# Performance work log

Hardware: AMD Instinct MI355X
Metric: run time of the kernel (lower is better)

The kernel has to match this reference:

```python
import jax, jax.numpy as jnp
import numpy as np

NUM_GROUPS = 32
EPS = 1e-6


def group_norm(x, scale, bias):
    # x: (b, c, t, h, w)
    b, c, t, h, w = x.shape
    xg = x.reshape(b, NUM_GROUPS, c // NUM_GROUPS, t, h, w)
    mean = jnp.mean(xg, axis=(2, 3, 4, 5), keepdims=True)
    var = jnp.var(xg, axis=(2, 3, 4, 5), keepdims=True)
    xg = (xg - mean) * jax.lax.rsqrt(var + EPS)
    xn = xg.reshape(b, c, t, h, w)
    return xn * scale[None, :, None, None, None] + bias[None, :, None, None, None]


def conv1x1(x, w, bvec):
    # 1x1x1 Conv3d == per-position linear over channels
    return jnp.einsum('oc,bcthw->bothw', w, x) + bvec[None, :, None, None, None]


def setup_inputs() -> dict:
    key = jax.random.key(0)
    ks = jax.random.split(key, 11)
    b, c, t, h, w = 2, 256, 4, 32, 32
    x = jax.random.normal(ks[0], (b, c, t, h, w), dtype=jnp.float32)
    s = 1.0 / np.sqrt(c)
    return {
        'x': x,
        'gn_scale': jnp.ones((c,), jnp.float32),
        'gn_bias': jnp.zeros((c,), jnp.float32),
        'wq': jax.random.normal(ks[1], (c, c), jnp.float32) * s,
        'bq': jax.random.normal(ks[2], (c,), jnp.float32) * 0.01,
        'wk': jax.random.normal(ks[3], (c, c), jnp.float32) * s,
        'bk': jax.random.normal(ks[4], (c,), jnp.float32) * 0.01,
        'wv': jax.random.normal(ks[5], (c, c), jnp.float32) * s,
        'bv': jax.random.normal(ks[6], (c,), jnp.float32) * 0.01,
        'wp': jax.random.normal(ks[7], (c, c), jnp.float32) * s,
        'bp': jax.random.normal(ks[8], (c,), jnp.float32) * 0.01,
    }


def reference(x, gn_scale, gn_bias, wq, bq, wk, bk, wv, bv, wp, bp):
    b, c, t, h, w = x.shape
    n = t * h * w
    h_ = group_norm(x, gn_scale, gn_bias)
    q = conv1x1(h_, wq, bq).reshape(b, c, n)  # (b, c, n)
    k = conv1x1(h_, wk, bk).reshape(b, c, n)
    v = conv1x1(h_, wv, bv).reshape(b, c, n)
    scale = jnp.asarray(int(c) ** (-0.5), x.dtype)
    # attn[b, i, j] = sum_c q[b,c,i] k[b,c,j]
    attn = jnp.einsum('bci,bcj->bij', q, k) * scale
    attn = jax.nn.softmax(attn, axis=2)
    # A[b, c, i] = sum_j v[b,c,j] attn[b,i,j]
    A = jnp.einsum('bcj,bij->bci', v, attn).reshape(b, c, t, h, w)
    A = conv1x1(A, wp, bp)
    return x + A
```

## Files before the change

### kernel.cpp

```cpp
#include <hip/hip_runtime.h>
#include <hip/hip_bf16.h>
#include <math.h>

#define BB 2
#define CC 256
#define GG 32
#define NN 4096
#define EPSF 1e-6f
#define JSPLIT 8
#define JBLK (NN / JSPLIT)
#define CH 32
#define NT (JBLK / CH)
#define QTILE 128
#define ITILE 32
#define LOG2E 1.4426950408889634f

typedef _Float16 f16x8 __attribute__((ext_vector_type(8)));
typedef float f32x4 __attribute__((ext_vector_type(4)));
typedef float f32x16 __attribute__((ext_vector_type(16)));

static __device__ __forceinline__ unsigned short f2h_bits(float f) {
    _Float16 h = (_Float16)f;
    return __builtin_bit_cast(unsigned short, h);
}
static __device__ __forceinline__ unsigned pkh2(float a, float b) {
    return __builtin_bit_cast(unsigned, __builtin_amdgcn_cvt_pkrtz(a, b));
}
static __device__ __forceinline__ void gload16(const void* g, void* l) {
    __builtin_amdgcn_global_load_lds(
        (const __attribute__((address_space(1))) void*)g,
        (__attribute__((address_space(3))) void*)l, 16, 0, 0);
}

__global__ __launch_bounds__(256) void prep_gn_kernel(
    const float* __restrict__ wq, const float* __restrict__ wk,
    const float* __restrict__ wv, const float* __restrict__ wp,
    unsigned short* __restrict__ w16,
    const float* __restrict__ x, float2* __restrict__ part)
{
    __shared__ float red[8];
    int id = blockIdx.x;
    int t  = threadIdx.x;
    if (id < 256) {
        int m = id >> 6;
        const float* src = (m == 0) ? wq : (m == 1) ? wk : (m == 2) ? wv : wp;
        float scale = (m == 0) ? 0.0625f * LOG2E : 1.0f;
        int idx = (id & 63) * 256 + t;
        float4 v = ((const float4*)src)[idx];
        union { _Float16 h[4]; uint2 u; } pk;
        pk.h[0] = (_Float16)(v.x * scale);
        pk.h[1] = (_Float16)(v.y * scale);
        pk.h[2] = (_Float16)(v.z * scale);
        pk.h[3] = (_Float16)(v.w * scale);
        *(uint2*)(w16 + (size_t)m * CC * CC + (size_t)idx * 4) = pk.u;
    } else {
        int rem = id - 256;
        int g = rem & 31, p = (rem >> 5) & 3, b = rem >> 7;
        const float* base = x + ((size_t)b * CC + (size_t)g * 8) * NN + (size_t)p * 8192;
        float s = 0.f, ss = 0.f;
        for (int idx = t; idx < 2048; idx += 256) {
            float4 v4 = ((const float4*)base)[idx];
            s  += v4.x + v4.y + v4.z + v4.w;
            ss += v4.x*v4.x + v4.y*v4.y + v4.z*v4.z + v4.w*v4.w;
        }
        for (int off = 32; off; off >>= 1) {
            s  += __shfl_down(s,  off);
            ss += __shfl_down(ss, off);
        }
        int wid = t >> 6;
        if ((t & 63) == 0) { red[wid*2] = s; red[wid*2+1] = ss; }
        __syncthreads();
        if (t == 0) {
            part[(b*GG + g)*4 + p] = make_float2(red[0]+red[2]+red[4]+red[6],
                                                 red[1]+red[3]+red[5]+red[7]);
        }
    }
}

__global__ __launch_bounds__(256) void proj_qkv_kernel(
    const float* __restrict__ x, const float* __restrict__ sc,
    const float* __restrict__ bi, const float2* __restrict__ part,
    const unsigned short* __restrict__ w16,
    const float* __restrict__ bq, const float* __restrict__ bk,
    const float* __restrict__ bv,
    unsigned short* __restrict__ qT, unsigned short* __restrict__ kT,
    unsigned short* __restrict__ vC)
{
    int b  = blockIdx.y;
    int i0 = blockIdx.x * 32;
    int t  = threadIdx.x;
    __shared__ unsigned short htile[32 * 256];
    __shared__ float s_mean[GG], s_rstd[GG], s_sc[CC], s_bi[CC];
    if (t < GG) {
        float2 p0 = part[(b*GG + t)*4 + 0];
        float2 p1 = part[(b*GG + t)*4 + 1];
        float2 p2 = part[(b*GG + t)*4 + 2];
        float2 p3 = part[(b*GG + t)*4 + 3];
        float S  = p0.x + p1.x + p2.x + p3.x;
        float SS = p0.y + p1.y + p2.y + p3.y;
        float mean = S / 32768.f;
        float var  = SS / 32768.f - mean * mean;
        s_mean[t] = mean;
        s_rstd[t] = rsqrtf(var + EPSF);
    }
    s_sc[t] = sc[t];
    s_bi[t] = bi[t];
    __syncthreads();

    char* hw = (char*)htile;
    int nq = (t & 7) * 4;
    int cq = (t >> 3) * 4;
    #pragma unroll
    for (int k = 0; k < 2; k++) {
        int c0 = cq + k * 128;
        float4 xr[4];
        float aa[4], dd[4];
        #pragma unroll
        for (int e = 0; e < 4; e++) {
            int c = c0 + e;
            xr[e] = *(const float4*)(x + ((size_t)b*CC + c)*NN + i0 + nq);
            aa[e] = s_rstd[c >> 3] * s_sc[c];
            dd[e] = s_bi[c] - s_mean[c >> 3] * aa[e];
        }
        #pragma unroll
        for (int j = 0; j < 4; j++) {
            int row = nq + j;
            union { _Float16 h[4]; uint2 u; } pk;
            pk.h[0] = (_Float16)(((const float*)&xr[0])[j] * aa[0] + dd[0]);
            pk.h[1] = (_Float16)(((const float*)&xr[1])[j] * aa[1] + dd[1]);
            pk.h[2] = (_Float16)(((const float*)&xr[2])[j] * aa[2] + dd[2]);
            pk.h[3] = (_Float16)(((const float*)&xr[3])[j] * aa[3] + dd[3]);
            int off = row*512 + (((c0 >> 3) ^ (row & 7)) << 4) + (c0 & 7) * 2;
            *(uint2*)(hw + off) = pk.u;
        }
    }
    __syncthreads();

    int lane = t & 63, w = t >> 6;
    int col = lane & 15, grp = lane >> 4;
    const char* hr = (const char*)htile;

    #pragma unroll
    for (int p = 0; p < 2; p++) {
        const unsigned short* wgt = w16 + (size_t)p * CC * CC;
        const float* bias = p ? bk : bq;
        unsigned short* outp = (p ? kT : qT) + (size_t)b * NN * CC;
        float osc = p ? 1.0f : 0.0625f * LOG2E;
        #pragma unroll
        for (int ot = 0; ot < 4; ot++) {
            int ow = ot * 64 + w * 16;
            f32x4 acc[2];
            acc[0] = (f32x4){0.f,0.f,0.f,0.f};
            acc[1] = (f32x4){0.f,0.f,0.f,0.f};
            #pragma unroll
            for (int ck = 0; ck < 8; ck++) {
                f16x8 af = *(const f16x8*)(wgt + (size_t)(ow + col)*CC + ck*32 + grp*8);
                #pragma unroll
                for (int it = 0; it < 2; it++) {
                    int row = it*16 + col;
                    f16x8 bf = *(const f16x8*)(hr + row*512 + (((ck*4 + grp) ^ (row & 7)) << 4));
                    acc[it] = __builtin_amdgcn_mfma_f32_16x16x32_f16(af, bf, acc[it], 0, 0, 0);
                }
            }
            int obase = ow + grp * 4;
            float b0 = bias[obase]*osc, b1 = bias[obase+1]*osc,
                  b2 = bias[obase+2]*osc, b3 = bias[obase+3]*osc;
            #pragma unroll
            for (int it = 0; it < 2; it++) {
                int i = i0 + it*16 + col;
                union { _Float16 h[4]; uint2 u; } pk;
                pk.h[0] = (_Float16)(acc[it][0] + b0);
                pk.h[1] = (_Float16)(acc[it][1] + b1);
                pk.h[2] = (_Float16)(acc[it][2] + b2);
                pk.h[3] = (_Float16)(acc[it][3] + b3);
                *(uint2*)(outp + (size_t)i*CC + obase) = pk.u;
            }
        }
    }
    {
        const unsigned short* wgt = w16 + (size_t)2 * CC * CC;
        unsigned short* outp = vC + (size_t)b * CC * NN;
        int ibase = (w & 1) * 16;
        #pragma unroll
        for (int gg = 0; gg < 2; gg++) {
            int og = (w >> 1) * 2 + gg;
            f32x4 acc[4];
            #pragma unroll
            for (int ot = 0; ot < 4; ot++) acc[ot] = (f32x4){0.f,0.f,0.f,0.f};
            #pragma unroll
            for (int ck = 0; ck < 8; ck++) {
                int row = ibase + col;
                f16x8 af = *(const f16x8*)(hr + row*512 + (((ck*4 + grp) ^ (row & 7)) << 4));
                #pragma unroll
                for (int ot = 0; ot < 4; ot++) {
                    f16x8 bf = *(const f16x8*)(wgt + (size_t)(og*64 + ot*16 + col)*CC + ck*32 + grp*8);
                    acc[ot] = __builtin_amdgcn_mfma_f32_16x16x32_f16(af, bf, acc[ot], 0, 0, 0);
                }
            }
            int iw = i0 + ibase + grp * 4;
            #pragma unroll
            for (int ot = 0; ot < 4; ot++) {
                int o = og*64 + ot*16 + col;
                float bo = bv[o];
                union { _Float16 h[4]; uint2 u; } pk;
                pk.h[0] = (_Float16)(acc[ot][0] + bo);
                pk.h[1] = (_Float16)(acc[ot][1] + bo);
                pk.h[2] = (_Float16)(acc[ot][2] + bo);
                pk.h[3] = (_Float16)(acc[ot][3] + bo);
                *(uint2*)(outp + (size_t)o*NN + iw) = pk.u;
            }
        }
    }
}

#define STAGE_K(tt, bb) do { int _j = jlo + (tt)*CH; _Pragma("unroll") \
    for (int e = 0; e < 4; e++) gload16(kb + (size_t)_j*CC + koff[e], &bufK[bb][(4*w + e)*512]); } while (0)
#define STAGE_V(tt, bb) do { int _j = jlo + (tt)*CH; _Pragma("unroll") \
    for (int e = 0; e < 4; e++) gload16(vb + voff[e] + _j, &bufV[bb][(4*w + e)*512]); } while (0)

__global__ __launch_bounds__(256, 2) void attn_kernel(
    const unsigned short* __restrict__ qT,
    const unsigned short* __restrict__ kT,
    const unsigned short* __restrict__ vC,
    unsigned short* __restrict__ pO,
    float2* __restrict__ ml)
{
    int qt = blockIdx.x, s = blockIdx.y, b = blockIdx.z;
    int tid = threadIdx.x, w = tid >> 6, lane = tid & 63;
    int l31 = lane & 31, hi = lane >> 5;
    int col = lane & 15, grp = lane >> 4;
    int q0 = qt * QTILE + w * 32;
    int jlo = s * JBLK;

    __shared__ __align__(16) unsigned short bufK[2][8192];
    __shared__ __align__(16) unsigned short bufV[2][8192];
    __shared__ __align__(16) unsigned short plds[4 * 1280];

    const unsigned short* qb = qT + (size_t)b * NN * CC;
    const unsigned short* kb = kT + (size_t)b * NN * CC;
    const unsigned short* vb = vC + (size_t)b * CC * NN;

    f16x8 qf[16];
    #pragma unroll
    for (int ck = 0; ck < 16; ck++)
        qf[ck] = *(const f16x8*)(qb + (size_t)(q0 + l31)*CC + ck*16 + hi*8);

    int koff[4], voff[4];
    #pragma unroll
    for (int e = 0; e < 4; e++) {
        int blk = (4*w + e)*64 + lane;
        int kj = blk >> 5, kcb = blk & 31;
        koff[e] = kj*CC + ((kcb ^ (kj & 7)) * 8);
        int vc = blk >> 2, vcb = blk & 3;
        voff[e] = vc*NN + ((vcb ^ ((vc >> 1) & 3)) * 8);
    }
    int kru = l31 * 512;
    int kx  = l31 & 7;
    int vrb = col*64 + ((grp ^ ((col >> 1) & 3)) << 4);
    char* pw  = (char*)plds + w*2560 + l31*80 + 8*hi;
    const char* prd = (const char*)plds + w*2560;

    f32x4 O0[16], O1[16];
    #pragma unroll
    for (int ct = 0; ct < 16; ct++) {
        O0[ct] = (f32x4){0.f,0.f,0.f,0.f};
        O1[ct] = (f32x4){0.f,0.f,0.f,0.f};
    }
    float m = -1e30f, l = 0.f;

    STAGE_K(0, 0);
    STAGE_V(0, 0);
    __syncthreads();

    for (int t = 0; t < NT; t++) {
        int cur = t & 1;
        if (t + 1 < NT) {
            STAGE_K(t + 1, cur ^ 1);
            STAGE_V(t + 1, cur ^ 1);
        }
        const char* kbase = (const char*)&bufK[cur][0];
        const char* vbase = (const char*)&bufV[cur][0];

        f32x16 S;
        #pragma unroll
        for (int r = 0; r < 16; r++) S[r] = 0.f;
        __builtin_amdgcn_s_setprio(1);
        #pragma unroll
        for (int ck = 0; ck < 16; ck++) {
            f16x8 kf = *(const f16x8*)(kbase + kru + ((((ck*2) | hi) ^ kx) << 4));
            S = __builtin_amdgcn_mfma_f32_32x32x16_f16(kf, qf[ck], S, 0, 0, 0);
        }
        __builtin_amdgcn_s_setprio(0);

        float x0 = fmaxf(fmaxf(S[0], S[1]), fmaxf(S[2], S[3]));
        float x1 = fmaxf(fmaxf(S[4], S[5]), fmaxf(S[6], S[7]));
        float x2 = fmaxf(fmaxf(S[8], S[9]), fmaxf(S[10], S[11]));
        float x3 = fmaxf(fmaxf(S[12], S[13]), fmaxf(S[14], S[15]));
        float mh = fmaxf(fmaxf(x0, x1), fmaxf(x2, x3));
        float mx = fmaxf(mh, __shfl_xor(mh, 32));

        if (!__all(mx <= m + 8.f)) {
            float mn = fmaxf(m, mx);
            float f = exp2f(m - mn);
            m = mn;
            l *= f;
            float fq0 = __shfl(f, col);
            float fq1 = __shfl(f, 16 + col);
            #pragma unroll
            for (int ct = 0; ct < 16; ct++) { O0[ct] *= fq0; O1[ct] *= fq1; }
        }

        #pragma unroll
        for (int r = 0; r < 16; r++) S[r] = exp2f(S[r] - m);
        float ps = (((S[0]+S[1]) + (S[2]+S[3])) + ((S[4]+S[5]) + (S[6]+S[7])))
                 + (((S[8]+S[9]) + (S[10]+S[11])) + ((S[12]+S[13]) + (S[14]+S[15])));
        l += ps + __shfl_xor(ps, 32);

        {
            unsigned* pr = (unsigned*)pw;
            pr[0]  = pkh2(S[0],  S[1]);   pr[1]  = pkh2(S[2],  S[3]);
            pr[4]  = pkh2(S[4],  S[5]);   pr[5]  = pkh2(S[6],  S[7]);
            pr[8]  = pkh2(S[8],  S[9]);   pr[9]  = pkh2(S[10], S[11]);
            pr[12] = pkh2(S[12], S[13]);  pr[13] = pkh2(S[14], S[15]);
        }
        asm volatile("s_waitcnt lgkmcnt(0)" ::: "memory");
        __builtin_amdgcn_sched_barrier(0);

        f16x8 y0 = *(const f16x8*)(prd + col*80 + grp*16);
        f16x8 y1 = *(const f16x8*)(prd + (16 + col)*80 + grp*16);
        __builtin_amdgcn_s_setprio(1);
        #pragma unroll
        for (int ct = 0; ct < 16; ct++) {
            f16x8 xf = *(const f16x8*)(vbase + ct*1024 + vrb);
            O0[ct] = __builtin_amdgcn_mfma_f32_16x16x32_f16(xf, y0, O0[ct], 0, 0, 0);
            O1[ct] = __builtin_amdgcn_mfma_f32_16x16x32_f16(xf, y1, O1[ct], 0, 0, 0);
        }
        __builtin_amdgcn_s_setprio(0);
        __syncthreads();
    }

    float inv = 1.f / l;
    float iq0 = __shfl(inv, col);
    float iq1 = __shfl(inv, 16 + col);
    unsigned short* po = pO + ((size_t)(s*BB + b)*NN + q0) * CC;
    #pragma unroll
    for (int ct = 0; ct < 16; ct++) {
        int c = ct*16 + grp*4;
        *(unsigned*)(po + (size_t)col*CC + c)            = pkh2(O0[ct][0]*iq0, O0[ct][1]*iq0);
        *(unsigned*)(po + (size_t)col*CC + c + 2)        = pkh2(O0[ct][2]*iq0, O0[ct][3]*iq0);
        *(unsigned*)(po + (size_t)(16 + col)*CC + c)     = pkh2(O1[ct][0]*iq1, O1[ct][1]*iq1);
        *(unsigned*)(po + (size_t)(16 + col)*CC + c + 2) = pkh2(O1[ct][2]*iq1, O1[ct][3]*iq1);
    }
    if (lane < 32)
        ml[(size_t)(s*BB + b)*NN + q0 + lane] = make_float2(m, l);
}

__global__ __launch_bounds__(256, 2) void proj_out_merge_kernel(
    const unsigned short* __restrict__ pO, const float2* __restrict__ ml,
    const unsigned short* __restrict__ wp16, const float* __restrict__ bp,
    const float* __restrict__ x, float* __restrict__ out)
{
    int b  = blockIdx.y;
    int i0 = blockIdx.x * ITILE;
    int t  = threadIdx.x;
    __shared__ __align__(16) unsigned short htile[ITILE * 256];

    {
        int row  = t >> 3;
        int cseg = (t & 7) * 32;
        size_t qrow = (size_t)b * NN + i0 + row;
        float M = -1e30f;
        float m8[JSPLIT], l8[JSPLIT];
        #pragma unroll
        for (int s = 0; s < JSPLIT; s++) {
            float2 v = ml[(size_t)s*BB*NN + qrow];
            m8[s] = v.x; l8[s] = v.y;
            M = fmaxf(M, v.x);
        }
        float W = 0.f, wt[JSPLIT];
        #pragma unroll
        for (int s = 0; s < JSPLIT; s++) { wt[s] = l8[s] * exp2f(m8[s] - M); W += wt[s]; }
        float iW = 1.f / W;
        float acc[32];
        #pragma unroll
        for (int e = 0; e < 32; e++) acc[e] = 0.f;
        #pragma unroll
        for (int s = 0; s < JSPLIT; s++) {
            const unsigned short* p = pO + ((size_t)s*BB*NN + qrow)*CC + cseg;
            float ws = wt[s] * iW;
            #pragma unroll
            for (int k = 0; k < 4; k++) {
                f16x8 a = *(const f16x8*)(p + k*8);
                #pragma unroll
                for (int e = 0; e < 8; e++) acc[k*8 + e] += ws * (float)a[e];
            }
        }
        char* hw = (char*)htile;
        #pragma unroll
        for (int k = 0; k < 4; k++) {
            int c0 = cseg + k*8;
            uint4 pk;
            pk.x = pkh2(acc[k*8+0], acc[k*8+1]);
            pk.y = pkh2(acc[k*8+2], acc[k*8+3]);
            pk.z = pkh2(acc[k*8+4], acc[k*8+5]);
            pk.w = pkh2(acc[k*8+6], acc[k*8+7]);
            int off = row*512 + (((c0 >> 3) ^ (row & 7)) << 4);
            *(uint4*)(hw + off) = pk;
        }
    }
    __syncthreads();

    int lane = t & 63, wid = t >> 6;
    int col = lane & 15, grp = lane >> 4;
    int rl0 = (wid & 1) * 16;
    int ibase = i0 + rl0;
    const char* hr = (const char*)htile;
    #pragma unroll
    for (int gg = 0; gg < 2; gg++) {
        int o0 = ((wid >> 1) * 2 + gg) * 64;
        f32x4 acc[4];
        #pragma unroll
        for (int ot = 0; ot < 4; ot++) acc[ot] = (f32x4){0.f,0.f,0.f,0.f};
        #pragma unroll
        for (int ck = 0; ck < 8; ck++) {
            int rl = rl0 + col;
            f16x8 af = *(const f16x8*)(hr + rl*512 + (((ck*4 + grp) ^ (rl & 7)) << 4));
            #pragma unroll
            for (int ot = 0; ot < 4; ot++) {
                f16x8 bf = *(const f16x8*)(wp16 + (size_t)(o0 + ot*16 + col)*CC + ck*32 + grp*8);
                acc[ot] = __builtin_amdgcn_mfma_f32_16x16x32_f16(af, bf, acc[ot], 0, 0, 0);
            }
        }
        int iw = ibase + grp * 4;
        #pragma unroll
        for (int ot = 0; ot < 4; ot++) {
            int o = o0 + ot*16 + col;
            float bo = bp[o];
            size_t base = (size_t)b*CC*NN + (size_t)o*NN + iw;
            float4 x4 = *(const float4*)(x + base);
            float4 r;
            r.x = x4.x + acc[ot][0] + bo;
            r.y = x4.y + acc[ot][1] + bo;
            r.z = x4.z + acc[ot][2] + bo;
            r.w = x4.w + acc[ot][3] + bo;
            *(float4*)(out + base) = r;
        }
    }
}

extern "C" void kernel_launch(void* const* d_in, const int* in_sizes, int n_in,
                              void* d_out, int out_size, void* d_ws, size_t ws_size,
                              hipStream_t stream) {
    const float* x  = (const float*)d_in[0];
    const float* gs = (const float*)d_in[1];
    const float* gb = (const float*)d_in[2];
    const float* wq = (const float*)d_in[3];
    const float* bq = (const float*)d_in[4];
    const float* wk = (const float*)d_in[5];
    const float* bk = (const float*)d_in[6];
    const float* wv = (const float*)d_in[7];
    const float* bv = (const float*)d_in[8];
    const float* wp = (const float*)d_in[9];
    const float* bp = (const float*)d_in[10];
    float* out = (float*)d_out;

    char* ws = (char*)d_ws;
    const size_t sz = (size_t)BB * NN * CC * sizeof(unsigned short);
    unsigned short* qT  = (unsigned short*)(ws + sz);
    unsigned short* kT  = (unsigned short*)(ws + 2*sz);
    unsigned short* vC  = (unsigned short*)(ws + 3*sz);
    unsigned short* w16 = (unsigned short*)(ws + 5*sz);
    float2* part        = (float2*)(ws + 5*sz + 512*1024);
    float2* ml          = (float2*)(ws + 5*sz + 768*1024);
    unsigned short* pO  = (unsigned short*)(ws + 5*sz + 1280*1024);

    prep_gn_kernel<<<dim3(512), 256, 0, stream>>>(wq, wk, wv, wp, w16, x, part);
    proj_qkv_kernel<<<dim3(NN/32, BB), 256, 0, stream>>>(x, gs, gb, part, w16,
                                                         bq, bk, bv, qT, kT, vC);
    attn_kernel<<<dim3(NN/QTILE, JSPLIT, BB), 256, 0, stream>>>(qT, kT, vC, pO, ml);
    proj_out_merge_kernel<<<dim3(NN/ITILE, BB), 256, 0, stream>>>(pO, ml, w16 + 3*CC*CC,
                                                                  bp, x, out);
}
```

Measured before the change: 116.9 us.

## Software-pipeline QK^T one tile ahead with triple-buffered K in attention

The attention kernel now uses 512 threads per block covering a 256-row query tile, so each block's staged K/V tiles feed twice as many query rows and each thread issues half as many async loads. K is triple-buffered and V double-buffered. The QK^T MFMA for tile t+1 is computed before the softmax and PV of tile t, so matrix work overlaps the softmax and the global-to-LDS waits. Explicit vmcnt waits and raw s_barrier calls replace __syncthreads. The costs are more registers (S2 is held live alongside the O accumulators), more LDS per block and fewer blocks in the grid, which may reduce occupancy on the chip.

```diff
diff --git a/kernel.cpp b/kernel.cpp
--- a/kernel.cpp
+++ b/kernel.cpp
@@ -11,7 +11,7 @@
 #define JBLK (NN / JSPLIT)
 #define CH 32
 #define NT (JBLK / CH)
-#define QTILE 128
+#define QTILE 256
 #define ITILE 32
 #define LOG2E 1.4426950408889634f
 
@@ -31,6 +31,9 @@
         (const __attribute__((address_space(1))) void*)g,
         (__attribute__((address_space(3))) void*)l, 16, 0, 0);
 }
+#define WAITV(n) asm volatile("s_waitcnt vmcnt(" #n ")" ::: "memory")
+#define SBAR() do { __builtin_amdgcn_sched_barrier(0); __builtin_amdgcn_s_barrier(); \
+                    __builtin_amdgcn_sched_barrier(0); } while (0)
 
 __global__ __launch_bounds__(256) void prep_gn_kernel(
     const float* __restrict__ wq, const float* __restrict__ wk,
@@ -214,11 +217,17 @@
 }
 
 #define STAGE_K(tt, bb) do { int _j = jlo + (tt)*CH; _Pragma("unroll") \
-    for (int e = 0; e < 4; e++) gload16(kb + (size_t)_j*CC + koff[e], &bufK[bb][(4*w + e)*512]); } while (0)
+    for (int e = 0; e < 2; e++) gload16(kb + (size_t)_j*CC + koff[e], &bufK[bb][(2*w + e)*512]); } while (0)
 #define STAGE_V(tt, bb) do { int _j = jlo + (tt)*CH; _Pragma("unroll") \
-    for (int e = 0; e < 4; e++) gload16(vb + voff[e] + _j, &bufV[bb][(4*w + e)*512]); } while (0)
-
-__global__ __launch_bounds__(256, 2) void attn_kernel(
+    for (int e = 0; e < 2; e++) gload16(vb + voff[e] + _j, &bufV[bb][(2*w + e)*512]); } while (0)
+#define QK_INTO(dst, kn) do { \
+    _Pragma("unroll") for (int r = 0; r < 16; r++) dst[r] = 0.f; \
+    _Pragma("unroll") for (int ck = 0; ck < 16; ck++) { \
+        f16x8 kf = *(const f16x8*)((kn) + kru + ((((ck*2) | hi) ^ kx) << 4)); \
+        dst = __builtin_amdgcn_mfma_f32_32x32x16_f16(kf, qf[ck], dst, 0, 0, 0); \
+    } } while (0)
+
+__global__ __launch_bounds__(512, 2) void attn_kernel(
     const unsigned short* __restrict__ qT,
     const unsigned short* __restrict__ kT,
     const unsigned short* __restrict__ vC,
@@ -232,9 +241,9 @@
     int q0 = qt * QTILE + w * 32;
     int jlo = s * JBLK;
 
-    __shared__ __align__(16) unsigned short bufK[2][8192];
+    __shared__ __align__(16) unsigned short bufK[3][8192];
     __shared__ __align__(16) unsigned short bufV[2][8192];
-    __shared__ __align__(16) unsigned short plds[4 * 1280];
+    __shared__ __align__(16) unsigned short plds[8 * 1280];
 
     const unsigned short* qb = qT + (size_t)b * NN * CC;
     const unsigned short* kb = kT + (size_t)b * NN * CC;
@@ -245,10 +254,10 @@
     for (int ck = 0; ck < 16; ck++)
         qf[ck] = *(const f16x8*)(qb + (size_t)(q0 + l31)*CC + ck*16 + hi*8);
 
-    int koff[4], voff[4];
-    #pragma unroll
-    for (int e = 0; e < 4; e++) {
-        int blk = (4*w + e)*64 + lane;
+    int koff[2], voff[2];
+    #pragma unroll
+    for (int e = 0; e < 2; e++) {
+        int blk = (2*w + e)*64 + lane;
         int kj = blk >> 5, kcb = blk & 31;
         koff[e] = kj*CC + ((kcb ^ (kj & 7)) * 8);
         int vc = blk >> 2, vcb = blk & 3;
@@ -268,29 +277,32 @@
     }
     float m = -1e30f, l = 0.f;
 
+    STAGE_V(0, 0);
     STAGE_K(0, 0);
-    STAGE_V(0, 0);
-    __syncthreads();
+    STAGE_K(1, 1);
+    WAITV(2);
+    SBAR();
+
+    f32x16 S;
+    {
+        const char* kn = (const char*)&bufK[0][0];
+        QK_INTO(S, kn);
+    }
 
     for (int t = 0; t < NT; t++) {
-        int cur = t & 1;
+        if (t + 1 < NT) STAGE_V(t + 1, (t + 1) & 1);
+        if (t + 2 < NT) STAGE_K(t + 2, (t + 2) % 3);
         if (t + 1 < NT) {
-            STAGE_K(t + 1, cur ^ 1);
-            STAGE_V(t + 1, cur ^ 1);
-        }
-        const char* kbase = (const char*)&bufK[cur][0];
-        const char* vbase = (const char*)&bufV[cur][0];
-
-        f32x16 S;
-        #pragma unroll
-        for (int r = 0; r < 16; r++) S[r] = 0.f;
+            if (t + 2 < NT) { WAITV(4); } else { WAITV(2); }
+            SBAR();
+        }
+
         __builtin_amdgcn_s_setprio(1);
-        #pragma unroll
-        for (int ck = 0; ck < 16; ck++) {
-            f16x8 kf = *(const f16x8*)(kbase + kru + ((((ck*2) | hi) ^ kx) << 4));
-            S = __builtin_amdgcn_mfma_f32_32x32x16_f16(kf, qf[ck], S, 0, 0, 0);
-        }
-        __builtin_amdgcn_s_setprio(0);
+        f32x16 S2;
+        if (t + 1 < NT) {
+            const char* kn = (const char*)&bufK[(t + 1) % 3][0];
+            QK_INTO(S2, kn);
+        }
 
         float x0 = fmaxf(fmaxf(S[0], S[1]), fmaxf(S[2], S[3]));
         float x1 = fmaxf(fmaxf(S[4], S[5]), fmaxf(S[6], S[7]));
@@ -328,7 +340,7 @@
 
         f16x8 y0 = *(const f16x8*)(prd + col*80 + grp*16);
         f16x8 y1 = *(const f16x8*)(prd + (16 + col)*80 + grp*16);
-        __builtin_amdgcn_s_setprio(1);
+        const char* vbase = (const char*)&bufV[t & 1][0];
         #pragma unroll
         for (int ct = 0; ct < 16; ct++) {
             f16x8 xf = *(const f16x8*)(vbase + ct*1024 + vrb);
@@ -336,7 +348,12 @@
             O1[ct] = __builtin_amdgcn_mfma_f32_16x16x32_f16(xf, y1, O1[ct], 0, 0, 0);
         }
         __builtin_amdgcn_s_setprio(0);
-        __syncthreads();
+
+        if (t + 1 < NT) {
+            if (t + 2 < NT) { WAITV(2); } else { WAITV(0); }
+            SBAR();
+            S = S2;
+        }
     }
 
     float inv = 1.f / l;
@@ -477,7 +494,7 @@
     prep_gn_kernel<<<dim3(512), 256, 0, stream>>>(wq, wk, wv, wp, w16, x, part);
     proj_qkv_kernel<<<dim3(NN/32, BB), 256, 0, stream>>>(x, gs, gb, part, w16,
                                                          bq, bk, bv, qT, kT, vC);
-    attn_kernel<<<dim3(NN/QTILE, JSPLIT, BB), 256, 0, stream>>>(qT, kT, vC, pO, ml);
+    attn_kernel<<<dim3(NN/QTILE, JSPLIT, BB), 512, 0, stream>>>(qT, kT, vC, pO, ml);
     proj_out_merge_kernel<<<dim3(NN/ITILE, BB), 256, 0, stream>>>(pO, ml, w16 + 3*CC*CC,
                                                                   bp, x, out);
 }
```

New measurement: 140.0 us. 19.8% more time.
